# Kernel optimization log

Hardware: AMD Instinct MI355X
Metric: run time of the kernel (lower is better)

The kernel has to match this reference:

```python
import jax, jax.numpy as jnp
import numpy as np

PATCH = 64      # patch generator patch size
LD = 1.0        # self.ld
WS = 11         # SSIM gaussian window size
SIGMA = 1.5
C1 = 0.01 ** 2
C2 = 0.03 ** 2


def _gauss_window(channels):
    x = jnp.arange(WS, dtype=jnp.float32)
    g = jnp.exp(-((x - WS // 2) ** 2) / (2.0 * SIGMA * SIGMA))
    g = g / g.sum()
    w2 = jnp.outer(g, g)               # (WS, WS), sums to 1
    return jnp.broadcast_to(w2[None, None], (channels, 1, WS, WS))


def _dwconv(x, w, channels):
    # depthwise 'same' conv, padding = WS//2 (matches F.conv2d(..., padding=ws//2, groups=C))
    p = WS // 2
    return jax.lax.conv_general_dilated(
        x, w, window_strides=(1, 1), padding=[(p, p), (p, p)],
        dimension_numbers=("NCHW", "OIHW", "NCHW"), feature_group_count=channels)


def _ssim(img1, img2):
    # img1, img2: (n, C, h, w) -> per-image mean SSIM, shape (n,)
    ch = img1.shape[1]
    w = _gauss_window(ch).astype(img1.dtype)
    mu1 = _dwconv(img1, w, ch)
    mu2 = _dwconv(img2, w, ch)
    mu1_sq, mu2_sq, mu1_mu2 = mu1 * mu1, mu2 * mu2, mu1 * mu2
    sigma1_sq = _dwconv(img1 * img1, w, ch) - mu1_sq
    sigma2_sq = _dwconv(img2 * img2, w, ch) - mu2_sq
    sigma12 = _dwconv(img1 * img2, w, ch) - mu1_mu2
    ssim_map = ((2.0 * mu1_mu2 + C1) * (2.0 * sigma12 + C2)) / (
        (mu1_sq + mu2_sq + C1) * (sigma1_sq + sigma2_sq + C2))
    return jnp.mean(ssim_map, axis=(1, 2, 3))


def _to_patches(x, ps):
    # (B, C, H, W) -> (B, P, C, ps, ps) with P = (H//ps)*(W//ps)
    B, C, H, W = x.shape
    x = x.reshape(B, C, H // ps, ps, W // ps, ps)
    x = x.transpose(0, 2, 4, 1, 3, 5)
    return x.reshape(B, (H // ps) * (W // ps), C, ps, ps)


def setup_inputs() -> dict:
    key = jax.random.key(0)
    ks = jax.random.split(key, 5)
    shp = (32, 3, 512, 512)
    names = ["A", "N", "GT", "G", "BG"]
    return {n: jax.random.uniform(k, shp, dtype=jnp.float32) for n, k in zip(names, ks)}


def reference(A, N, GT, G, BG):
    pA = _to_patches(A, PATCH)
    pN = _to_patches(N, PATCH)
    pGT = _to_patches(GT, PATCH)
    pG = _to_patches(G, PATCH)
    pBG = _to_patches(BG, PATCH)
    B, P, C, h, w = pA.shape
    # batched SSIM over all (B*P) patches (replaces the python double loop)
    ssim_scores = _ssim(pN.reshape(B * P, C, h, w), pGT.reshape(B * P, C, h, w)).reshape(B, P)
    diff = jnp.minimum(LD * (1.0 - ssim_scores), jnp.ones_like(ssim_scores))
    bg_loss = jnp.mean((pBG - pG) ** 2, axis=(2, 3, 4))
    a_loss = jnp.mean((pA - pG) ** 2, axis=(2, 3, 4))
    loss = diff * bg_loss + (1.0 - diff) * a_loss
    return jnp.sum(loss)
```

## Files before the change

### kernel.cpp

```cpp
#include <hip/hip_runtime.h>
#include <math.h>

#define C1C 1e-4f
#define C2C 9e-4f

#define GW0 0.00102838f
#define GW1 0.00759876f
#define GW2 0.03600077f
#define GW3 0.10936069f
#define GW4 0.21300554f
#define GW5 0.26601173f
__device__ __forceinline__ float conv11(const float* w) {
    float a = GW0 * (w[0] + w[10]);
    a = fmaf(GW1, w[1] + w[9], a);
    a = fmaf(GW2, w[2] + w[8], a);
    a = fmaf(GW3, w[3] + w[7], a);
    a = fmaf(GW4, w[4] + w[6], a);
    a = fmaf(GW5, w[5], a);
    return a;
}

#define SROWS 74
#define SSTR  36

__global__ __launch_bounds__(256, 3) void ssim_fused_kernel(
    const float* __restrict__ A,  const float* __restrict__ Nimg,
    const float* __restrict__ GT, const float* __restrict__ G,
    const float* __restrict__ BG,
    float* __restrict__ ssim_sum, float* __restrict__ sa_sum,
    float* __restrict__ sbg_sum)
{
    __shared__ float S0[SROWS][SSTR];
    __shared__ float S1[SROWS][SSTR];
    __shared__ float S2[SROWS][SSTR];
    __shared__ float S3[SROWS][SSTR];

    const int q  = blockIdx.x;
    const int c  = blockIdx.y;
    const int b  = q >> 6;
    const int pp = q & 63;
    const int ph = pp >> 3;
    const int pw = pp & 7;
    const unsigned base = ((unsigned)(b * 3 + c) << 18)
                        + ((unsigned)(ph * 64) << 9)
                        + (unsigned)(pw * 64);
    const int t = threadIdx.x;

    for (int i = t; i < 10 * SSTR; i += 256) {
        const int r  = i / SSTR;
        const int cc = i - r * SSTR;
        const int rr = (r < 5) ? r : 64 + r;
        S0[rr][cc] = 0.f; S1[rr][cc] = 0.f;
        S2[rr][cc] = 0.f; S3[rr][cc] = 0.f;
    }

    const int hr   = t >> 2;
    const int hseg = t & 3;
    const int c0   = hseg << 3;
    const unsigned rowBase = base + ((unsigned)hr << 9);
    const int vcol = t & 31;
    const int vr0  = (t >> 5) << 3;

    float accS = 0.f;

    for (int h = 0; h < 2; ++h) {
        const int g0 = (h << 5) + c0;
        float s[18], d[18];
        #pragma unroll
        for (int m = 0; m < 6; ++m) {
            const int cb = g0 - 8 + 4 * m;
            float4 xv = make_float4(0.f, 0.f, 0.f, 0.f);
            float4 yv = make_float4(0.f, 0.f, 0.f, 0.f);
            if (cb >= 0 && cb < 64) {
                xv = *(const float4*)(Nimg + rowBase + cb);
                yv = *(const float4*)(GT   + rowBase + cb);
            }
            #pragma unroll
            for (int u = 0; u < 4; ++u) {
                const int j = 4 * m + u - 3;
                if (j >= 0 && j < 18) {
                    s[j] = (&xv.x)[u] + (&yv.x)[u];
                    d[j] = (&xv.x)[u] - (&yv.x)[u];
                }
            }
        }

        #pragma unroll
        for (int mm = 0; mm < 2; ++mm) {
            float4 o;
            #pragma unroll
            for (int u = 0; u < 4; ++u) (&o.x)[u] = conv11(&s[4*mm + u]);
            *(float4*)&S2[5 + hr][c0 + 4*mm] = o;
        }
        #pragma unroll
        for (int i = 0; i < 18; ++i) s[i] = s[i] * s[i];
        #pragma unroll
        for (int mm = 0; mm < 2; ++mm) {
            float4 o;
            #pragma unroll
            for (int u = 0; u < 4; ++u) (&o.x)[u] = conv11(&s[4*mm + u]);
            *(float4*)&S0[5 + hr][c0 + 4*mm] = o;
        }
        #pragma unroll
        for (int mm = 0; mm < 2; ++mm) {
            float4 o;
            #pragma unroll
            for (int u = 0; u < 4; ++u) (&o.x)[u] = conv11(&d[4*mm + u]);
            *(float4*)&S3[5 + hr][c0 + 4*mm] = o;
        }
        #pragma unroll
        for (int i = 0; i < 18; ++i) d[i] = d[i] * d[i];
        #pragma unroll
        for (int mm = 0; mm < 2; ++mm) {
            float4 o;
            #pragma unroll
            for (int u = 0; u < 4; ++u) (&o.x)[u] = conv11(&d[4*mm + u]);
            *(float4*)&S1[5 + hr][c0 + 4*mm] = o;
        }
        __syncthreads();

        {
            float t2[8], ss[8], uv[8];
            float w[18];
            #pragma unroll
            for (int dd = 0; dd < 18; ++dd) w[dd] = S2[vr0 + dd][vcol];
            #pragma unroll
            for (int o = 0; o < 8; ++o) t2[o] = conv11(&w[o]);
            #pragma unroll
            for (int dd = 0; dd < 18; ++dd) w[dd] = S3[vr0 + dd][vcol];
            #pragma unroll
            for (int o = 0; o < 8; ++o) {
                const float bb = conv11(&w[o]);
                const float A2 = t2[o] * t2[o];
                const float B2 = bb * bb;
                t2[o] = 0.5f * (A2 - B2);
                ss[o] = 0.5f * (A2 + B2);
            }
            #pragma unroll
            for (int dd = 0; dd < 18; ++dd) w[dd] = S0[vr0 + dd][vcol];
            #pragma unroll
            for (int o = 0; o < 8; ++o) uv[o] = conv11(&w[o]);
            #pragma unroll
            for (int dd = 0; dd < 18; ++dd) w[dd] = S1[vr0 + dd][vcol];
            #pragma unroll
            for (int o = 0; o < 8; ++o) {
                const float vvv  = conv11(&w[o]);
                const float numL = t2[o] + C1C;
                const float denL = ss[o] + C1C;
                const float numR = fmaf(0.5f, uv[o] - vvv, C2C - t2[o]);
                const float denR = fmaf(0.5f, uv[o] + vvv, C2C - ss[o]);
                accS += (numL * numR) * __builtin_amdgcn_rcpf(denL * denR);
            }
        }
        __syncthreads();
    }

    float sa = 0.f, sbg = 0.f;
    #pragma unroll
    for (int it = 0; it < 4; ++it) {
        const int idx  = t + 256 * it;
        const int row  = idx >> 4;
        const int col4 = (idx & 15) << 2;
        const unsigned off = base + ((unsigned)row << 9) + col4;
        const float4 av  = *(const float4*)(A  + off);
        const float4 gv  = *(const float4*)(G  + off);
        const float4 bgv = *(const float4*)(BG + off);
        float d0 = bgv.x - gv.x, d1 = bgv.y - gv.y, d2 = bgv.z - gv.z, d3 = bgv.w - gv.w;
        sbg += d0*d0 + d1*d1 + d2*d2 + d3*d3;
        float e0 = av.x - gv.x, e1 = av.y - gv.y, e2 = av.z - gv.z, e3 = av.w - gv.w;
        sa  += e0*e0 + e1*e1 + e2*e2 + e3*e3;
    }

    #pragma unroll
    for (int off = 32; off; off >>= 1) {
        accS += __shfl_down(accS, off, 64);
        sa   += __shfl_down(sa,   off, 64);
        sbg  += __shfl_down(sbg,  off, 64);
    }
    const int wv = t >> 6;
    if ((t & 63) == 0) {
        S0[0][wv] = accS; S0[1][wv] = sa; S0[2][wv] = sbg;
    }
    __syncthreads();
    if (t == 0) {
        const int plane = q * 3 + c;
        ssim_sum[plane] = S0[0][0] + S0[0][1] + S0[0][2] + S0[0][3];
        sa_sum[plane]   = S0[1][0] + S0[1][1] + S0[1][2] + S0[1][3];
        sbg_sum[plane]  = S0[2][0] + S0[2][1] + S0[2][2] + S0[2][3];
    }
}

__global__ __launch_bounds__(256) void combine_kernel(
    const float* __restrict__ ssim_sum, const float* __restrict__ sa_sum,
    const float* __restrict__ sbg_sum, float* __restrict__ out)
{
    __shared__ float red[4];
    const int t = threadIdx.x;
    const float invN = 1.f / 12288.f;
    float acc = 0.f;
    #pragma unroll
    for (int r = 0; r < 8; ++r) {
        const int qq = t + 256 * r;
        const float ss = ssim_sum[3*qq] + ssim_sum[3*qq+1] + ssim_sum[3*qq+2];
        const float sa = sa_sum[3*qq]   + sa_sum[3*qq+1]   + sa_sum[3*qq+2];
        const float sb = sbg_sum[3*qq]  + sbg_sum[3*qq+1]  + sbg_sum[3*qq+2];
        const float ssim = ss * invN;
        const float diff = fminf(1.f - ssim, 1.f);
        acc += diff * (sb * invN) + (1.f - diff) * (sa * invN);
    }
    #pragma unroll
    for (int off = 32; off; off >>= 1) acc += __shfl_down(acc, off, 64);
    if ((t & 63) == 0) red[t >> 6] = acc;
    __syncthreads();
    if (t == 0) out[0] = red[0] + red[1] + red[2] + red[3];
}

extern "C" void kernel_launch(void* const* d_in, const int* in_sizes, int n_in,
                              void* d_out, int out_size, void* d_ws, size_t ws_size,
                              hipStream_t stream) {
    const float* A  = (const float*)d_in[0];
    const float* Nn = (const float*)d_in[1];
    const float* GT = (const float*)d_in[2];
    const float* G  = (const float*)d_in[3];
    const float* BG = (const float*)d_in[4];
    float* out      = (float*)d_out;

    float* ssim_sum = (float*)d_ws;
    float* sa_sum   = ssim_sum + 6144;
    float* sbg_sum  = ssim_sum + 12288;

    ssim_fused_kernel<<<dim3(2048, 3), 256, 0, stream>>>(
        A, Nn, GT, G, BG, ssim_sum, sa_sum, sbg_sum);
    combine_kernel<<<1, 256, 0, stream>>>(ssim_sum, sa_sum, sbg_sum, out);
}
```

Measured before the change: 434.7 us.

## Use 128-thread blocks with narrower 16-column strips and 2x4 vertical outputs

Halves the block to 128 threads and processes each 64x64 patch in four 16-column strips instead of two 32-column strips, shrinking shared memory per block. In the vertical pass each thread now reads float2 pairs over 14 rows and produces a 2x4 output tile, cutting LDS reads per output compared with 18 scalar reads for 8 outputs. The intent is higher occupancy from smaller LDS use and less LDS traffic. The cost is twice as many barriers and loop iterations per block, and fewer threads per block to hide global load latency.

```diff
diff --git a/kernel.cpp b/kernel.cpp
--- a/kernel.cpp
+++ b/kernel.cpp
@@ -21,9 +21,9 @@
 }
 
 #define SROWS 74
-#define SSTR  36
-
-__global__ __launch_bounds__(256, 3) void ssim_fused_kernel(
+#define SSTR  20
+
+__global__ __launch_bounds__(128, 3) void ssim_fused_kernel(
     const float* __restrict__ A,  const float* __restrict__ Nimg,
     const float* __restrict__ GT, const float* __restrict__ G,
     const float* __restrict__ BG,
@@ -46,7 +46,7 @@
                         + (unsigned)(pw * 64);
     const int t = threadIdx.x;
 
-    for (int i = t; i < 10 * SSTR; i += 256) {
+    for (int i = t; i < 10 * SSTR; i += 128) {
         const int r  = i / SSTR;
         const int cc = i - r * SSTR;
         const int rr = (r < 5) ? r : 64 + r;
@@ -54,17 +54,16 @@
         S2[rr][cc] = 0.f; S3[rr][cc] = 0.f;
     }
 
-    const int hr   = t >> 2;
-    const int hseg = t & 3;
-    const int c0   = hseg << 3;
+    const int hr = t >> 1;
+    const int hg = (t & 1) << 3;
     const unsigned rowBase = base + ((unsigned)hr << 9);
-    const int vcol = t & 31;
-    const int vr0  = (t >> 5) << 3;
+    const int vp  = (t & 7) << 1;
+    const int vr0 = (t >> 3) << 2;
 
     float accS = 0.f;
 
-    for (int h = 0; h < 2; ++h) {
-        const int g0 = (h << 5) + c0;
+    for (int h = 0; h < 4; ++h) {
+        const int g0 = (h << 4) + hg;
         float s[18], d[18];
         #pragma unroll
         for (int m = 0; m < 6; ++m) {
@@ -90,7 +89,7 @@
             float4 o;
             #pragma unroll
             for (int u = 0; u < 4; ++u) (&o.x)[u] = conv11(&s[4*mm + u]);
-            *(float4*)&S2[5 + hr][c0 + 4*mm] = o;
+            *(float4*)&S2[5 + hr][hg + 4*mm] = o;
         }
         #pragma unroll
         for (int i = 0; i < 18; ++i) s[i] = s[i] * s[i];
@@ -99,14 +98,14 @@
             float4 o;
             #pragma unroll
             for (int u = 0; u < 4; ++u) (&o.x)[u] = conv11(&s[4*mm + u]);
-            *(float4*)&S0[5 + hr][c0 + 4*mm] = o;
+            *(float4*)&S0[5 + hr][hg + 4*mm] = o;
         }
         #pragma unroll
         for (int mm = 0; mm < 2; ++mm) {
             float4 o;
             #pragma unroll
             for (int u = 0; u < 4; ++u) (&o.x)[u] = conv11(&d[4*mm + u]);
-            *(float4*)&S3[5 + hr][c0 + 4*mm] = o;
+            *(float4*)&S3[5 + hr][hg + 4*mm] = o;
         }
         #pragma unroll
         for (int i = 0; i < 18; ++i) d[i] = d[i] * d[i];
@@ -115,50 +114,80 @@
             float4 o;
             #pragma unroll
             for (int u = 0; u < 4; ++u) (&o.x)[u] = conv11(&d[4*mm + u]);
-            *(float4*)&S1[5 + hr][c0 + 4*mm] = o;
+            *(float4*)&S1[5 + hr][hg + 4*mm] = o;
         }
         __syncthreads();
 
         {
+            float w0[14], w1[14];
             float t2[8], ss[8], uv[8];
-            float w[18];
-            #pragma unroll
-            for (int dd = 0; dd < 18; ++dd) w[dd] = S2[vr0 + dd][vcol];
-            #pragma unroll
-            for (int o = 0; o < 8; ++o) t2[o] = conv11(&w[o]);
-            #pragma unroll
-            for (int dd = 0; dd < 18; ++dd) w[dd] = S3[vr0 + dd][vcol];
-            #pragma unroll
-            for (int o = 0; o < 8; ++o) {
-                const float bb = conv11(&w[o]);
-                const float A2 = t2[o] * t2[o];
-                const float B2 = bb * bb;
+            #pragma unroll
+            for (int dd = 0; dd < 14; ++dd) {
+                const float2 rv = *(const float2*)&S2[vr0 + dd][vp];
+                w0[dd] = rv.x; w1[dd] = rv.y;
+            }
+            #pragma unroll
+            for (int o = 0; o < 4; ++o) {
+                t2[o]     = conv11(&w0[o]);
+                t2[4 + o] = conv11(&w1[o]);
+            }
+            #pragma unroll
+            for (int dd = 0; dd < 14; ++dd) {
+                const float2 rv = *(const float2*)&S3[vr0 + dd][vp];
+                w0[dd] = rv.x; w1[dd] = rv.y;
+            }
+            #pragma unroll
+            for (int o = 0; o < 4; ++o) {
+                float bb = conv11(&w0[o]);
+                float A2 = t2[o] * t2[o], B2 = bb * bb;
                 t2[o] = 0.5f * (A2 - B2);
                 ss[o] = 0.5f * (A2 + B2);
-            }
-            #pragma unroll
-            for (int dd = 0; dd < 18; ++dd) w[dd] = S0[vr0 + dd][vcol];
-            #pragma unroll
-            for (int o = 0; o < 8; ++o) uv[o] = conv11(&w[o]);
-            #pragma unroll
-            for (int dd = 0; dd < 18; ++dd) w[dd] = S1[vr0 + dd][vcol];
-            #pragma unroll
-            for (int o = 0; o < 8; ++o) {
-                const float vvv  = conv11(&w[o]);
+                bb = conv11(&w1[o]);
+                A2 = t2[4+o] * t2[4+o]; B2 = bb * bb;
+                t2[4+o] = 0.5f * (A2 - B2);
+                ss[4+o] = 0.5f * (A2 + B2);
+            }
+            #pragma unroll
+            for (int dd = 0; dd < 14; ++dd) {
+                const float2 rv = *(const float2*)&S0[vr0 + dd][vp];
+                w0[dd] = rv.x; w1[dd] = rv.y;
+            }
+            #pragma unroll
+            for (int o = 0; o < 4; ++o) {
+                uv[o]     = conv11(&w0[o]);
+                uv[4 + o] = conv11(&w1[o]);
+            }
+            #pragma unroll
+            for (int dd = 0; dd < 14; ++dd) {
+                const float2 rv = *(const float2*)&S1[vr0 + dd][vp];
+                w0[dd] = rv.x; w1[dd] = rv.y;
+            }
+            #pragma unroll
+            for (int o = 0; o < 4; ++o) {
+                const float vvv  = conv11(&w0[o]);
                 const float numL = t2[o] + C1C;
                 const float denL = ss[o] + C1C;
                 const float numR = fmaf(0.5f, uv[o] - vvv, C2C - t2[o]);
                 const float denR = fmaf(0.5f, uv[o] + vvv, C2C - ss[o]);
                 accS += (numL * numR) * __builtin_amdgcn_rcpf(denL * denR);
             }
+            #pragma unroll
+            for (int o = 0; o < 4; ++o) {
+                const float vvv  = conv11(&w1[o]);
+                const float numL = t2[4+o] + C1C;
+                const float denL = ss[4+o] + C1C;
+                const float numR = fmaf(0.5f, uv[4+o] - vvv, C2C - t2[4+o]);
+                const float denR = fmaf(0.5f, uv[4+o] + vvv, C2C - ss[4+o]);
+                accS += (numL * numR) * __builtin_amdgcn_rcpf(denL * denR);
+            }
         }
         __syncthreads();
     }
 
     float sa = 0.f, sbg = 0.f;
     #pragma unroll
-    for (int it = 0; it < 4; ++it) {
-        const int idx  = t + 256 * it;
+    for (int it = 0; it < 8; ++it) {
+        const int idx  = t + 128 * it;
         const int row  = idx >> 4;
         const int col4 = (idx & 15) << 2;
         const unsigned off = base + ((unsigned)row << 9) + col4;
@@ -184,9 +213,9 @@
     __syncthreads();
     if (t == 0) {
         const int plane = q * 3 + c;
-        ssim_sum[plane] = S0[0][0] + S0[0][1] + S0[0][2] + S0[0][3];
-        sa_sum[plane]   = S0[1][0] + S0[1][1] + S0[1][2] + S0[1][3];
-        sbg_sum[plane]  = S0[2][0] + S0[2][1] + S0[2][2] + S0[2][3];
+        ssim_sum[plane] = S0[0][0] + S0[0][1];
+        sa_sum[plane]   = S0[1][0] + S0[1][1];
+        sbg_sum[plane]  = S0[2][0] + S0[2][1];
     }
 }
 
@@ -229,7 +258,7 @@
     float* sa_sum   = ssim_sum + 6144;
     float* sbg_sum  = ssim_sum + 12288;
 
-    ssim_fused_kernel<<<dim3(2048, 3), 256, 0, stream>>>(
+    ssim_fused_kernel<<<dim3(2048, 3), 128, 0, stream>>>(
         A, Nn, GT, G, BG, ssim_sum, sa_sum, sbg_sum);
     combine_kernel<<<1, 256, 0, stream>>>(ssim_sum, sa_sum, sbg_sum, out);
 }
```

Result: slower. 476.1 us (+9.5%).
